# Kernel tuning notes

Hardware: AMD Instinct MI355X
Metric: run time of the kernel (lower is better)

## Reference

```python
import jax, jax.numpy as jnp
import numpy as np


def setup_inputs() -> dict:
    key = jax.random.key(0)
    k1, k2, k3, k4 = jax.random.split(key, 4)
    B, T, E, H = 16, 2048, 1024, 128
    x = jax.random.normal(k1, (B, T, E), dtype=jnp.float32)
    Wk = jax.random.normal(k2, (E, H), dtype=jnp.float32) * (E ** -0.5)
    Wq = jax.random.normal(k3, (E, H), dtype=jnp.float32) * (E ** -0.5)
    Wv = jax.random.normal(k4, (E, H), dtype=jnp.float32) * (E ** -0.5)
    return {"x": x, "Wk": Wk, "Wq": Wq, "Wv": Wv}


def reference(x, Wk, Wq, Wv):
    # x: [B,T,E]; Wk/Wq/Wv: [E,H]
    B, T, E = x.shape
    H = Wk.shape[1]
    k = jnp.einsum('bte,eh->bth', x, Wk)
    q = jnp.einsum('bte,eh->bth', x, Wq)
    v = jnp.einsum('bte,eh->bth', x, Wv)
    # scores [B,T,T]; original masks with -inf THEN scales (equivalent math)
    scores = jnp.einsum('bqh,bkh->bqk', q, k) * (H ** -0.5)
    causal = jnp.tril(jnp.ones((T, T), dtype=bool))
    scores = jnp.where(causal, scores, -jnp.inf)
    weights = jax.nn.softmax(scores, axis=-1)
    # dropout disabled (eval mode reference)
    return jnp.einsum('bqk,bkh->bqh', weights, v)
```

## Files before the change

kernel.cpp:

```cpp
#include <hip/hip_runtime.h>

#define B_ 16
#define T_ 2048
#define E_ 1024
#define H_ 128

typedef short bf16x8 __attribute__((ext_vector_type(8)));
typedef float f32x4 __attribute__((ext_vector_type(4)));
typedef unsigned short u16x4 __attribute__((ext_vector_type(4)));

static __device__ __forceinline__ unsigned short f2bf(float f) {
    unsigned int u = __float_as_uint(f);
    u += 0x7FFFu + ((u >> 16) & 1u);
    return (unsigned short)(u >> 16);
}
static __device__ __forceinline__ unsigned int pk2(unsigned short a, unsigned short b) {
    return (unsigned int)a | ((unsigned int)b << 16);
}
static __device__ __forceinline__ bf16x8 frag(uint4 v) {
    return __builtin_bit_cast(bf16x8, v);
}

__global__ __launch_bounds__(256) void wcvt_kernel(
    const float* __restrict__ w0, const float* __restrict__ w1,
    const float* __restrict__ w2, unsigned short* __restrict__ wt)
{
    int g   = blockIdx.x * 256 + threadIdx.x;
    int arr = g >> 14;
    int rem = g & 16383;
    int h   = rem >> 7;
    int e0  = (rem & 127) * 8;
    const float* src = (arr == 0) ? w0 : (arr == 1) ? w1 : w2;
    unsigned short b[8];
#pragma unroll
    for (int i = 0; i < 8; i++) b[i] = f2bf(src[(size_t)(e0 + i) * H_ + h]);
    uint4 o;
    o.x = pk2(b[0], b[1]); o.y = pk2(b[2], b[3]);
    o.z = pk2(b[4], b[5]); o.w = pk2(b[6], b[7]);
    size_t off = ((size_t)(e0 >> 5) * 384 + arr * 128 + h) * 32 + (e0 & 31);
    *(uint4*)&wt[off] = o;
}

__global__ __launch_bounds__(384, 3) void proj_kernel(
    const float* __restrict__ x,
    const unsigned short* __restrict__ wt,
    unsigned short* __restrict__ q_ws,
    unsigned short* __restrict__ k_ws,
    unsigned short* __restrict__ vt_ws)
{
    const int m0    = blockIdx.x * 128;
    const int nbase = blockIdx.y * 192;
    __shared__ __align__(16) unsigned short Xs[128][40];
    __shared__ __align__(16) unsigned short Wl[192][40];

    const int tid  = threadIdx.x;
    const int lane = tid & 63;
    const int w    = tid >> 6;
    const int quad = lane >> 4;
    const int lm   = lane & 15;
    const int rw   = (w & 1) * 64;
    const int cw   = (w >> 1) * 64;

    const f32x4 z4 = {0.f, 0.f, 0.f, 0.f};
    f32x4 acc[4][4];
#pragma unroll
    for (int i = 0; i < 4; i++)
#pragma unroll
        for (int j = 0; j < 4; j++) acc[i][j] = z4;

    for (int kb = 0; kb < 32; kb++) {
        const int k0 = kb * 32;
        __syncthreads();
#pragma unroll
        for (int j = 0; j < 2; j++) {
            int idx = j * 384 + tid;
            if (idx < 512) {
                int row = idx >> 2, c = (idx & 3) * 8;
                const float* xp = x + (size_t)(m0 + row) * E_ + k0 + c;
                float4 a = *(const float4*)xp;
                float4 b = *(const float4*)(xp + 4);
                uint4 u;
                u.x = pk2(f2bf(a.x), f2bf(a.y));
                u.y = pk2(f2bf(a.z), f2bf(a.w));
                u.z = pk2(f2bf(b.x), f2bf(b.y));
                u.w = pk2(f2bf(b.z), f2bf(b.w));
                *(uint4*)&Xs[row][c] = u;
            }
        }
#pragma unroll
        for (int j = 0; j < 2; j++) {
            int fl = (j * 384 + tid) * 8;
            int nl = fl >> 5, kk = fl & 31;
            *(uint4*)&Wl[nl][kk] =
                *(const uint4*)&wt[((size_t)kb * 384 + nbase + nl) * 32 + kk];
        }
        __syncthreads();

        bf16x8 a[4], b[4];
#pragma unroll
        for (int am = 0; am < 4; am++)
            a[am] = frag(*(const uint4*)&Xs[rw + am * 16 + lm][quad * 8]);
#pragma unroll
        for (int bn = 0; bn < 4; bn++)
            b[bn] = frag(*(const uint4*)&Wl[cw + bn * 16 + lm][quad * 8]);
#pragma unroll
        for (int am = 0; am < 4; am++)
#pragma unroll
            for (int bn = 0; bn < 4; bn++)
                acc[am][bn] = __builtin_amdgcn_mfma_f32_16x16x32_bf16(
                    a[am], b[bn], acc[am][bn], 0, 0, 0);
    }

    const int bb = m0 >> 11;
    const int t0 = m0 & 2047;
#pragma unroll
    for (int am = 0; am < 4; am++)
#pragma unroll
        for (int bn = 0; bn < 4; bn++) {
            const int cg  = nbase + cw + bn * 16 + lm;
            const int row = m0 + rw + am * 16 + quad * 4;
            if (cg < 128) {
#pragma unroll
                for (int r = 0; r < 4; r++)
                    q_ws[(size_t)(row + r) * H_ + cg] = f2bf(acc[am][bn][r]);
            } else if (cg < 256) {
#pragma unroll
                for (int r = 0; r < 4; r++)
                    k_ws[(size_t)(row + r) * H_ + (cg - 128)] = f2bf(acc[am][bn][r]);
            } else {
                const int h  = cg - 256;
                const int tt = t0 + rw + am * 16 + quad * 4;
                u16x4 p;
#pragma unroll
                for (int r = 0; r < 4; r++) p[r] = f2bf(acc[am][bn][r]);
                *(u16x4*)&vt_ws[((size_t)(bb * 64 + (tt >> 5)) * 128 + h) * 32 + (tt & 31)] = p;
            }
        }
}

__global__ __launch_bounds__(128, 2) void attn_kernel(
    const unsigned short* __restrict__ q_ws,
    const unsigned short* __restrict__ k_ws,
    const unsigned short* __restrict__ vt_ws,
    float* __restrict__ out)
{
    const int batch = blockIdx.x & 15;
    const int pair  = blockIdx.x >> 4;

    __shared__ __align__(16) unsigned short Ps[2][16][40];
    __shared__ __align__(16) float Cb[64][40];

    const int tid  = threadIdx.x;
    const int lane = tid & 63;
    const int w    = tid >> 6;
    const int quad = lane >> 4;
    const int lm   = lane & 15;
    const float scale = 0.08838834764831845f;

    const size_t bq = (size_t)batch * T_ * H_;

    bf16x8 ones;
#pragma unroll
    for (int i = 0; i < 8; i++) ones[i] = (short)0x3F80;

    for (int half = 0; half < 2; half++) {
        const int t   = half ? (127 - pair) : pair;
        const int nkt = (t + 2) >> 1;

        bf16x8 qf[4];
#pragma unroll
        for (int h = 0; h < 4; h++)
            qf[h] = frag(*(const uint4*)(q_ws + bq +
                     (size_t)(t * 16 + lm) * H_ + h * 32 + quad * 8));

        const f32x4 z4 = {0.f, 0.f, 0.f, 0.f};
        f32x4 o[9];
#pragma unroll
        for (int f = 0; f < 9; f++) o[f] = z4;

        for (int kt = w; kt < nkt; kt += 2) {
            const int k0 = kt * 32;
            uint4 kr[2][4];
#pragma unroll
            for (int hf = 0; hf < 2; hf++)
#pragma unroll
                for (int h = 0; h < 4; h++)
                    kr[hf][h] = *(const uint4*)(k_ws + bq +
                        (size_t)(k0 + hf * 16 + lm) * H_ + h * 32 + quad * 8);
            uint4 vr[8];
#pragma unroll
            for (int f = 0; f < 8; f++)
                vr[f] = *(const uint4*)(vt_ws +
                    ((size_t)(batch * 64 + kt) * 128 + f * 16 + lm) * 32 + quad * 8);

            f32x4 st0 = z4, st1 = z4;
#pragma unroll
            for (int h = 0; h < 4; h++) {
                st0 = __builtin_amdgcn_mfma_f32_16x16x32_bf16(frag(kr[0][h]), qf[h], st0, 0, 0, 0);
                st1 = __builtin_amdgcn_mfma_f32_16x16x32_bf16(frag(kr[1][h]), qf[h], st1, 0, 0, 0);
            }
            const int qg = t * 16 + lm;
            u16x4 pa, pb;
#pragma unroll
            for (int r = 0; r < 4; r++) {
                int kv0 = k0 + quad * 4 + r;
                float e0 = __expf(st0[r] * scale);
                float e1 = __expf(st1[r] * scale);
                pa[r] = (kv0      <= qg) ? f2bf(e0) : (unsigned short)0;
                pb[r] = (kv0 + 16 <= qg) ? f2bf(e1) : (unsigned short)0;
            }
            *(u16x4*)&Ps[w][lm][quad * 4]      = pa;
            *(u16x4*)&Ps[w][lm][16 + quad * 4] = pb;
            bf16x8 pf = frag(*(const uint4*)&Ps[w][lm][quad * 8]);

#pragma unroll
            for (int f = 0; f < 8; f++)
                o[f] = __builtin_amdgcn_mfma_f32_16x16x32_bf16(pf, frag(vr[f]), o[f], 0, 0, 0);
            o[8] = __builtin_amdgcn_mfma_f32_16x16x32_bf16(pf, ones, o[8], 0, 0, 0);
        }

        __syncthreads();
        if (w == 1) {
#pragma unroll
            for (int f = 0; f < 9; f++) *(f32x4*)&Cb[lane][f * 4] = o[f];
        }
        __syncthreads();
        if (w == 0) {
#pragma unroll
            for (int f = 0; f < 9; f++) {
                f32x4 p = *(const f32x4*)&Cb[lane][f * 4];
                o[f] += p;
            }
            float* op = out + bq + (size_t)(t * 16) * H_;
#pragma unroll
            for (int r = 0; r < 4; r++) {
                float inv = 1.f / o[8][r];
#pragma unroll
                for (int f = 0; f < 8; f++)
                    op[(size_t)(quad * 4 + r) * H_ + f * 16 + lm] = o[f][r] * inv;
            }
        }
        __syncthreads();
    }
}

extern "C" void kernel_launch(void* const* d_in, const int* in_sizes, int n_in,
                              void* d_out, int out_size, void* d_ws, size_t ws_size,
                              hipStream_t stream)
{
    const float* x  = (const float*)d_in[0];
    const float* Wk = (const float*)d_in[1];
    const float* Wq = (const float*)d_in[2];
    const float* Wv = (const float*)d_in[3];
    float* out = (float*)d_out;

    const size_t MH = (size_t)B_ * T_ * H_;
    unsigned short* q_ws  = (unsigned short*)d_ws;
    unsigned short* k_ws  = q_ws + MH;
    unsigned short* vt_ws = k_ws + MH;
    unsigned short* wt    = vt_ws + MH;

    wcvt_kernel<<<dim3(192), dim3(256), 0, stream>>>(Wq, Wk, Wv, wt);
    proj_kernel<<<dim3(256, 2), dim3(384), 0, stream>>>(x, wt, q_ws, k_ws, vt_ws);
    attn_kernel<<<dim3(1024), dim3(128), 0, stream>>>(q_ws, k_ws, vt_ws, out);
}
```

Measured before the change: 333.8 us.

## Prefetch next K/V tiles into registers and remap batches onto XCDs

```diff
diff --git a/kernel.cpp b/kernel.cpp
--- a/kernel.cpp
+++ b/kernel.cpp
@@ -144,7 +144,8 @@
     const unsigned short* __restrict__ vt_ws,
     float* __restrict__ out)
 {
-    const int batch = blockIdx.x & 15;
+    const int xcd   = blockIdx.x & 7;
+    const int batch = xcd + 8 * ((blockIdx.x >> 3) & 1);
     const int pair  = blockIdx.x >> 4;
 
     __shared__ __align__(16) unsigned short Ps[2][16][40];
@@ -178,20 +179,24 @@
 #pragma unroll
         for (int f = 0; f < 9; f++) o[f] = z4;
 
+        uint4 kr[2][4], vr[8];
+        {
+            const int kp = (w < nkt) ? w * 32 : 0;
+            const int tp = kp >> 5;
+#pragma unroll
+            for (int hf = 0; hf < 2; hf++)
+#pragma unroll
+                for (int h = 0; h < 4; h++)
+                    kr[hf][h] = *(const uint4*)(k_ws + bq +
+                        (size_t)(kp + hf * 16 + lm) * H_ + h * 32 + quad * 8);
+#pragma unroll
+            for (int f = 0; f < 8; f++)
+                vr[f] = *(const uint4*)(vt_ws +
+                    ((size_t)(batch * 64 + tp) * 128 + f * 16 + lm) * 32 + quad * 8);
+        }
+
         for (int kt = w; kt < nkt; kt += 2) {
             const int k0 = kt * 32;
-            uint4 kr[2][4];
-#pragma unroll
-            for (int hf = 0; hf < 2; hf++)
-#pragma unroll
-                for (int h = 0; h < 4; h++)
-                    kr[hf][h] = *(const uint4*)(k_ws + bq +
-                        (size_t)(k0 + hf * 16 + lm) * H_ + h * 32 + quad * 8);
-            uint4 vr[8];
-#pragma unroll
-            for (int f = 0; f < 8; f++)
-                vr[f] = *(const uint4*)(vt_ws +
-                    ((size_t)(batch * 64 + kt) * 128 + f * 16 + lm) * 32 + quad * 8);
 
             f32x4 st0 = z4, st1 = z4;
 #pragma unroll
@@ -199,6 +204,23 @@
                 st0 = __builtin_amdgcn_mfma_f32_16x16x32_bf16(frag(kr[0][h]), qf[h], st0, 0, 0, 0);
                 st1 = __builtin_amdgcn_mfma_f32_16x16x32_bf16(frag(kr[1][h]), qf[h], st1, 0, 0, 0);
             }
+
+            uint4 krn[2][4], vrn[8];
+            {
+                const int ktn = (kt + 2 < nkt) ? kt + 2 : kt;
+                const int kn  = ktn * 32;
+#pragma unroll
+                for (int hf = 0; hf < 2; hf++)
+#pragma unroll
+                    for (int h = 0; h < 4; h++)
+                        krn[hf][h] = *(const uint4*)(k_ws + bq +
+                            (size_t)(kn + hf * 16 + lm) * H_ + h * 32 + quad * 8);
+#pragma unroll
+                for (int f = 0; f < 8; f++)
+                    vrn[f] = *(const uint4*)(vt_ws +
+                        ((size_t)(batch * 64 + ktn) * 128 + f * 16 + lm) * 32 + quad * 8);
+            }
+
             const int qg = t * 16 + lm;
             u16x4 pa, pb;
 #pragma unroll
@@ -217,6 +239,13 @@
             for (int f = 0; f < 8; f++)
                 o[f] = __builtin_amdgcn_mfma_f32_16x16x32_bf16(pf, frag(vr[f]), o[f], 0, 0, 0);
             o[8] = __builtin_amdgcn_mfma_f32_16x16x32_bf16(pf, ones, o[8], 0, 0, 0);
+
+#pragma unroll
+            for (int hf = 0; hf < 2; hf++)
+#pragma unroll
+                for (int h = 0; h < 4; h++) kr[hf][h] = krn[hf][h];
+#pragma unroll
+            for (int f = 0; f < 8; f++) vr[f] = vrn[f];
         }
 
         __syncthreads();
```

Result: no change. 337.5 us (+1.1%).
